# Performance work log

Measured on AMD Instinct MI355X. Metric: run time of the kernel, lower is better.

Reference implementation:

```python
import jax, jax.numpy as jnp
import numpy as np

H = 4096          # hidden_size
I = 11008         # intermediate_size
G = 128           # AWQ group_size
# AWQ interleaved nibble order within each packed int32
_ORDER = jnp.array([0, 4, 1, 5, 2, 6, 3, 7], dtype=jnp.int32) * 4


def _mk_lin(key, K, N):
    k1, k2, k3 = jax.random.split(key, 3)
    qw = jax.random.randint(k1, (K, N // 8), 0, 100, dtype=jnp.int32)
    qz = jax.random.randint(k2, (K // G, N // 8), 0, 100, dtype=jnp.int32)
    sc = jax.random.normal(k3, (K // G, N), dtype=jnp.float32) * 0.02
    return qw, qz, sc


def setup_inputs() -> dict:
    key = jax.random.key(0)
    ks = jax.random.split(key, 7)
    x = jax.random.normal(ks[0], (8, 16, H), dtype=jnp.float32)
    ln1_w = jnp.ones((H,), dtype=jnp.float32)
    ln2_w = jnp.ones((H,), dtype=jnp.float32)
    qkv_qw, qkv_qz, qkv_sc = _mk_lin(ks[1], H, 3 * H)
    o_qw, o_qz, o_sc = _mk_lin(ks[2], H, H)
    gu_qw, gu_qz, gu_sc = _mk_lin(ks[3], H, 2 * I)
    dn_qw, dn_qz, dn_sc = _mk_lin(ks[4], I, H)
    return dict(x=x, ln1_w=ln1_w, ln2_w=ln2_w,
                qkv_qw=qkv_qw, qkv_qz=qkv_qz, qkv_sc=qkv_sc,
                o_qw=o_qw, o_qz=o_qz, o_sc=o_sc,
                gu_qw=gu_qw, gu_qz=gu_qz, gu_sc=gu_sc,
                dn_qw=dn_qw, dn_qz=dn_qz, dn_sc=dn_sc)


def rmsnorm(x, w, eps=1e-6):
    return x * jax.lax.rsqrt(jnp.mean(x * x, axis=-1, keepdims=True) + eps) * w


def dequant(qw, qz, sc):
    # qw: [K, N//8] int32 -> [K, N]; qz: [K//G, N//8] -> [K//G, N]
    K = qw.shape[0]
    N = sc.shape[1]
    w = ((qw[:, :, None] >> _ORDER) & 0xF).reshape(K, N).astype(sc.dtype)
    z = ((qz[:, :, None] >> _ORDER) & 0xF).reshape(K // G, N).astype(sc.dtype)
    return (w - jnp.repeat(z, G, axis=0)) * jnp.repeat(sc, G, axis=0)


def lite_linear(x, qw, qz, sc):
    return x @ dequant(qw, qz, sc)


def reference(x, ln1_w, ln2_w,
              qkv_qw, qkv_qz, qkv_sc,
              o_qw, o_qz, o_sc,
              gu_qw, gu_qz, gu_sc,
              dn_qw, dn_qz, dn_sc):
    residual = x
    h = rmsnorm(x, ln1_w)
    h = lite_linear(h, qkv_qw, qkv_qz, qkv_sc)[..., :H]  # mock attn: take q slice
    h = lite_linear(h, o_qw, o_qz, o_sc)
    h = residual + h
    residual = h
    h = rmsnorm(h, ln2_w)
    gate_up = lite_linear(h, gu_qw, gu_qz, gu_sc)
    gate, up = gate_up[..., :I], gate_up[..., I:]
    h = lite_linear(jax.nn.silu(gate) * up, dn_qw, dn_qz, dn_sc)
    return residual + h
```

## Files before the change

kernel.cpp:

```cpp
#include <hip/hip_runtime.h>

typedef unsigned int   u32;
typedef unsigned short u16;

typedef _Float16 h2  __attribute__((ext_vector_type(2)));
typedef _Float16 h8  __attribute__((ext_vector_type(8)));
typedef float    f32x4 __attribute__((ext_vector_type(4)));

#define M_TOK 128

__device__ __forceinline__ u16 f2h_(float f) {
    _Float16 h = (_Float16)f; return __builtin_bit_cast(u16, h);
}
__device__ __forceinline__ float h2f_(u16 b) {
    _Float16 h = __builtin_bit_cast(_Float16, b); return (float)h;
}
__device__ __forceinline__ void acc8(uint4 v, float* s) {
#pragma unroll
    for (int i = 0; i < 4; ++i) {
        u32 w = ((const u32*)&v)[i];
        s[2 * i]     += h2f_((u16)(w & 0xFFFF));
        s[2 * i + 1] += h2f_((u16)(w >> 16));
    }
}

__constant__ int SHC[8] = {0, 16, 4, 20, 8, 24, 12, 28};

__launch_bounds__(256)
__global__ void pack_zs(const int* __restrict__ qz, const float* __restrict__ sc,
                        u32* __restrict__ zs, int qws, int scs, int Ncols, int total) {
    const int idx = blockIdx.x * 256 + threadIdx.x;
    if (idx >= total) return;
    const int g = idx / Ncols, n = idx - g * Ncols;
    const u32 d = (u32)qz[(size_t)g * qws + (n >> 3)];
    const u32 zj = (d >> SHC[n & 7]) & 15u;
    const u32 mz = 0xE400u | zj;
    const u16 sh = f2h_(sc[(size_t)g * scs + n]);
    zs[(size_t)g * Ncols + n] = mz | ((u32)sh << 16);
}


__launch_bounds__(256)
__global__ void rmsnorm_k(const float* __restrict__ in, const float* __restrict__ w,
                          u16* __restrict__ out) {
    const int row = blockIdx.x;
    const float* x = in + (size_t)row * 4096;
    float ss = 0.f;
#pragma unroll
    for (int j = 0; j < 16; ++j) {
        float v = x[threadIdx.x + 256 * j];
        ss += v * v;
    }
#pragma unroll
    for (int off = 32; off > 0; off >>= 1) ss += __shfl_down(ss, off, 64);
    __shared__ float ws4[4];
    if ((threadIdx.x & 63) == 0) ws4[threadIdx.x >> 6] = ss;
    __syncthreads();
    float total = ws4[0] + ws4[1] + ws4[2] + ws4[3];
    float r = rsqrtf(total * (1.f / 4096.f) + 1e-6f);
    const int mt = row >> 4, l16 = row & 15;
#pragma unroll
    for (int c2 = 0; c2 < 2; ++c2) {
        int c = threadIdx.x * 2 + c2;
        int kb = c >> 2, qq = c & 3;
        u16 o8[8];
#pragma unroll
        for (int j = 0; j < 8; ++j) {
            int i = c * 8 + j;
            o8[j] = f2h_(x[i] * r * w[i]);
        }
        *(uint4*)(out + ((size_t)(kb * 8 + mt) * 64 + qq * 16 + l16) * 8) = *(const uint4*)o8;
    }
}

__launch_bounds__(256, 3)
__global__ void gemm_awq(const u16* __restrict__ A, const u32* __restrict__ zs,
                         const int* __restrict__ qw, u16* __restrict__ part,
                         int qws, int N, int K, int kchunk) {
    __shared__ __align__(16) char lds[51200];

    const int tid = threadIdx.x, w = tid >> 6, lane = tid & 63;
    const int q = lane >> 4, l16 = lane & 15;
    const int nwg = gridDim.x, bid = blockIdx.x;
    const int qq8 = nwg >> 3, r8 = nwg & 7, xcd = bid & 7, boff = bid >> 3;
    const int bx = (xcd < r8 ? xcd * (qq8 + 1) : r8 * (qq8 + 1) + (xcd - r8) * qq8) + boff;
    const int n0w = bx * 128 + w * 32;
    const int pc0 = n0w >> 3;
    const int kp = lane & 31, h = lane >> 5;
    const int sk = blockIdx.y, kc0 = sk * kchunk, kend = min(kc0 + kchunk, K);

    char* ldsA0 = lds;
    char* ldsA1 = lds + 16384;
    char* myB   = lds + 32768 + w * 4608;
    const char* Ab = (const char*)A;
    const int stoff = w * 4096 + lane * 16;
    const int aoff  = (q * 16 + l16) * 16;
    const int* qws_base = qw + pc0;
    const u32* zsA = zs + n0w + h * 8;
    const u32* zsB = zs + n0w + 16 + h * 8;

    f32x4 acc[8][2] = {};
    uint4 za0, za1, zb0, zb1;

    auto ldraw = [&](int k0) -> uint4 {
        return *(const uint4*)(qws_base + (size_t)(k0 + lane) * qws);
    };
    auto loadzs = [&](int g) {
        za0 = *(const uint4*)(zsA + (size_t)g * N);
        za1 = *(const uint4*)(zsA + (size_t)g * N + 4);
        zb0 = *(const uint4*)(zsB + (size_t)g * N);
        zb1 = *(const uint4*)(zsB + (size_t)g * N + 4);
    };
    auto bperm8 = [&](uint4 rv, int* b) {
        const int i0 = kp * 8, i1 = i0 + 4;
        b[0] = __builtin_amdgcn_ds_bpermute(i0, (int)rv.x);
        b[1] = __builtin_amdgcn_ds_bpermute(i0, (int)rv.y);
        b[2] = __builtin_amdgcn_ds_bpermute(i0, (int)rv.z);
        b[3] = __builtin_amdgcn_ds_bpermute(i0, (int)rv.w);
        b[4] = __builtin_amdgcn_ds_bpermute(i1, (int)rv.x);
        b[5] = __builtin_amdgcn_ds_bpermute(i1, (int)rv.y);
        b[6] = __builtin_amdgcn_ds_bpermute(i1, (int)rv.z);
        b[7] = __builtin_amdgcn_ds_bpermute(i1, (int)rv.w);
    };
    auto emit_all = [&](const int* b, char* buf) {
        u32 qd0 = (u32)(h ? b[1] : b[0]);
        u32 qd1 = (u32)(h ? b[5] : b[4]);
        u32 qd2 = (u32)(h ? b[3] : b[2]);
        u32 qd3 = (u32)(h ? b[7] : b[6]);
        auto emit8 = [&](u32 w0, u32 w1, int nb, uint4 z0, uint4 z1) {
            char* bb = buf + kp * 4 + nb * 144;
            u32 w0s = w0 >> 4, w1s = w1 >> 4;
            auto em = [&](int j, u32 a0, u32 a1, int bsel, u32 zsj) {
                h2 mz = __builtin_bit_cast(h2, __builtin_amdgcn_perm(zsj, zsj, 0x01000100u));
                h2 s2 = __builtin_bit_cast(h2, __builtin_amdgcn_perm(zsj, zsj, 0x03020302u));
                u32 t = __builtin_amdgcn_perm(a1, a0, (u32)(bsel | ((bsel + 4) << 16)));
                u32 u = (t & 0x000F000Fu) | 0x64006400u;
                h2 v = (__builtin_bit_cast(h2, u) + mz) * s2;
                *(u32*)(bb + j * 144) = __builtin_bit_cast(u32, v);
            };
            em(0, w0, w1, 0, z0.x);  em(4, w0, w1, 1, z1.x);
            em(1, w0, w1, 2, z0.y);  em(5, w0, w1, 3, z1.y);
            em(2, w0s, w1s, 0, z0.z); em(6, w0s, w1s, 1, z1.z);
            em(3, w0s, w1s, 2, z0.w); em(7, w0s, w1s, 3, z1.w);
        };
        emit8(qd0, qd1, h * 8, za0, za1);
        emit8(qd2, qd3, 16 + h * 8, zb0, zb1);
    };

    loadzs(kc0 >> 7);
    uint4 rv0 = ldraw(kc0);
    uint4 rv_n = {0, 0, 0, 0};
    if (kc0 + 64 < kend) rv_n = ldraw(kc0 + 64);
    {
        const char* gs = Ab + (size_t)(kc0 >> 5) * 8192 + stoff;
        uint4 s0 = *(const uint4*)(gs);
        uint4 s1 = *(const uint4*)(gs + 1024);
        uint4 s2 = *(const uint4*)(gs + 2048);
        uint4 s3 = *(const uint4*)(gs + 3072);
        *(uint4*)(ldsA0 + stoff)        = s0;
        *(uint4*)(ldsA0 + stoff + 1024) = s1;
        *(uint4*)(ldsA0 + stoff + 2048) = s2;
        *(uint4*)(ldsA0 + stoff + 3072) = s3;
    }
    {
        int bp0[8];
        bperm8(rv0, bp0);
        emit_all(bp0, myB);
    }
    if (((kc0 + 64) & 127) == 0 && kc0 + 64 < kend)
        loadzs((kc0 + 64) >> 7);
    __syncthreads();

    char* cur = ldsA0; char* nxt = ldsA1;
    int bp[8];
    for (int k0 = kc0; k0 < kend; k0 += 64) {
        const bool kn1 = (k0 + 64) < kend, kn2 = (k0 + 128) < kend;
        uint4 s0 = {0,0,0,0}, s1 = {0,0,0,0}, s2 = {0,0,0,0}, s3 = {0,0,0,0};
        if (kn1) {
            const char* gs = Ab + (size_t)((k0 + 64) >> 5) * 8192 + stoff;
            s0 = *(const uint4*)(gs);
            s1 = *(const uint4*)(gs + 1024);
            s2 = *(const uint4*)(gs + 2048);
            s3 = *(const uint4*)(gs + 3072);
        }
        uint4 rv_f = {0, 0, 0, 0};
        if (kn2) rv_f = ldraw(k0 + 128);
        {
            uint4 bvc[2];
#pragma unroll
            for (int nt = 0; nt < 2; ++nt)
                bvc[nt] = *(const uint4*)(myB + (nt * 16 + l16) * 144 + q * 16);
            uint4 afc[8];
#pragma unroll
            for (int mt = 0; mt < 8; ++mt)
                afc[mt] = *(const uint4*)(cur + mt * 1024 + aoff);
            if (kn1) bperm8(rv_n, bp);
#pragma unroll
            for (int mt = 0; mt < 8; ++mt)
#pragma unroll
                for (int nt = 0; nt < 2; ++nt)
                    acc[mt][nt] = __builtin_amdgcn_mfma_f32_16x16x32_f16(
                        __builtin_bit_cast(h8, afc[mt]),
                        __builtin_bit_cast(h8, bvc[nt]),
                        acc[mt][nt], 0, 0, 0);
        }
        {
            uint4 bvc[2];
#pragma unroll
            for (int nt = 0; nt < 2; ++nt)
                bvc[nt] = *(const uint4*)(myB + (nt * 16 + l16) * 144 + 64 + q * 16);
            uint4 afc[8];
#pragma unroll
            for (int mt = 0; mt < 8; ++mt)
                afc[mt] = *(const uint4*)(cur + 8192 + mt * 1024 + aoff);
#pragma unroll
            for (int mt = 0; mt < 8; ++mt)
#pragma unroll
                for (int nt = 0; nt < 2; ++nt)
                    acc[mt][nt] = __builtin_amdgcn_mfma_f32_16x16x32_f16(
                        __builtin_bit_cast(h8, afc[mt]),
                        __builtin_bit_cast(h8, bvc[nt]),
                        acc[mt][nt], 0, 0, 0);
        }
        if (kn1) {
            emit_all(bp, myB);
            *(uint4*)(nxt + stoff)        = s0;
            *(uint4*)(nxt + stoff + 1024) = s1;
            *(uint4*)(nxt + stoff + 2048) = s2;
            *(uint4*)(nxt + stoff + 3072) = s3;
        }
        if (((k0 + 128) & 127) == 0 && (k0 + 128) < kend)
            loadzs((k0 + 128) >> 7);
        __syncthreads();
        rv_n = rv_f;
        char* t = cur; cur = nxt; nxt = t;
    }

    u16* pp = part + (size_t)sk * M_TOK * N;
#pragma unroll
    for (int mt = 0; mt < 8; ++mt)
#pragma unroll
        for (int nt = 0; nt < 2; ++nt) {
            const int n = n0w + nt * 16 + l16;
#pragma unroll
            for (int r = 0; r < 4; ++r) {
                const int m = mt * 16 + q * 4 + r;
                pp[(size_t)m * N + n] = f2h_(acc[mt][nt][r]);
            }
        }
}

__launch_bounds__(256)
__global__ void reduce_to_afrag(const u16* __restrict__ part, u16* __restrict__ out,
                                int SK) {
    const int idx = blockIdx.x * 256 + threadIdx.x;
    const int m = idx >> 9, c = idx & 511;
    float s[8] = {};
    for (int k = 0; k < SK; ++k)
        acc8(*(const uint4*)(part + (size_t)k * 524288 + (size_t)m * 4096 + c * 8), s);
    const int kb = c >> 2, qq = c & 3, mt = m >> 4, l16 = m & 15;
    u16 o8[8];
#pragma unroll
    for (int j = 0; j < 8; ++j) o8[j] = f2h_(s[j]);
    *(uint4*)(out + ((size_t)(kb * 8 + mt) * 64 + qq * 16 + l16) * 8) = *(const uint4*)o8;
}

__launch_bounds__(256)
__global__ void reduce_add_f32(const u16* __restrict__ part, const float* __restrict__ resin,
                               float* __restrict__ out, int SK) {
    const int idx = blockIdx.x * 256 + threadIdx.x;
    const size_t base = (size_t)idx * 8;
    float s[8];
    *(float4*)&s[0] = *(const float4*)(resin + base);
    *(float4*)&s[4] = *(const float4*)(resin + base + 4);
    for (int k = 0; k < SK; ++k)
        acc8(*(const uint4*)(part + (size_t)k * 524288 + base), s);
    *(float4*)(out + base)     = *(const float4*)&s[0];
    *(float4*)(out + base + 4) = *(const float4*)&s[4];
}

__launch_bounds__(256)
__global__ void silu_mul(const u16* __restrict__ part, u16* __restrict__ act, int SK) {
    const int idx = blockIdx.x * 256 + threadIdx.x;
    const int m = idx / 1376, c = idx - m * 1376;
    const int nb = c * 8;
    float g[8] = {}, u[8] = {};
    for (int k = 0; k < SK; ++k) {
        const size_t base = (size_t)k * 2818048 + (size_t)m * 22016 + nb;
        acc8(*(const uint4*)(part + base), g);
        acc8(*(const uint4*)(part + base + 11008), u);
    }
    const int kb = nb >> 5, qq = (nb >> 3) & 3, mt = m >> 4, l16 = m & 15;
    u16 o8[8];
#pragma unroll
    for (int j = 0; j < 8; ++j) {
        float a = g[j] / (1.f + __expf(-g[j])) * u[j];
        o8[j] = f2h_(a);
    }
    *(uint4*)(act + ((size_t)(kb * 8 + mt) * 64 + qq * 16 + l16) * 8) = *(const uint4*)o8;
}

extern "C" void kernel_launch(void* const* d_in, const int* in_sizes, int n_in,
                              void* d_out, int out_size, void* d_ws, size_t ws_size,
                              hipStream_t stream) {
    const float* x      = (const float*)d_in[0];
    const float* ln1_w  = (const float*)d_in[1];
    const float* ln2_w  = (const float*)d_in[2];
    const int*   qkv_qw = (const int*)d_in[3];
    const int*   qkv_qz = (const int*)d_in[4];
    const float* qkv_sc = (const float*)d_in[5];
    const int*   o_qw   = (const int*)d_in[6];
    const int*   o_qz   = (const int*)d_in[7];
    const float* o_sc   = (const float*)d_in[8];
    const int*   gu_qw  = (const int*)d_in[9];
    const int*   gu_qz  = (const int*)d_in[10];
    const float* gu_sc  = (const float*)d_in[11];
    const int*   dn_qw  = (const int*)d_in[12];
    const int*   dn_qz  = (const int*)d_in[13];
    const float* dn_sc  = (const float*)d_in[14];
    float* out = (float*)d_out;

    char* ws = (char*)d_ws;
    u16*   pbuf = (u16*)(ws);
    u32*   zsb  = (u32*)(ws + 45088768);
    u16*   act  = (u16*)(ws + 47906816);
    float* res2 = (float*)(ws + 50724864);
    u16*   slot = (u16*)(ws + 52822016);

    rmsnorm_k<<<128, 256, 0, stream>>>(x, ln1_w, slot);
    pack_zs<<<512, 256, 0, stream>>>(qkv_qz, qkv_sc, zsb, 1536, 12288, 4096, 131072);

    gemm_awq<<<dim3(32, 22), 256, 0, stream>>>(slot, zsb, qkv_qw, pbuf,
                                               1536, 4096, 4096, 192);
    reduce_to_afrag<<<256, 256, 0, stream>>>(pbuf, slot, 22);
    pack_zs<<<512, 256, 0, stream>>>(o_qz, o_sc, zsb, 512, 4096, 4096, 131072);

    gemm_awq<<<dim3(32, 22), 256, 0, stream>>>(slot, zsb, o_qw, pbuf,
                                               512, 4096, 4096, 192);
    reduce_add_f32<<<256, 256, 0, stream>>>(pbuf, x, res2, 22);

    rmsnorm_k<<<128, 256, 0, stream>>>(res2, ln2_w, slot);
    pack_zs<<<2752, 256, 0, stream>>>(gu_qz, gu_sc, zsb, 2752, 22016, 22016, 704512);

    gemm_awq<<<dim3(172, 5), 256, 0, stream>>>(slot, zsb, gu_qw, pbuf,
                                               2752, 22016, 4096, 832);
    silu_mul<<<688, 256, 0, stream>>>(pbuf, act, 5);
    pack_zs<<<1376, 256, 0, stream>>>(dn_qz, dn_sc, zsb, 512, 4096, 4096, 352256);

    gemm_awq<<<dim3(32, 25), 256, 0, stream>>>(act, zsb, dn_qw, pbuf,
                                               512, 4096, 11008, 448);
    reduce_add_f32<<<256, 256, 0, stream>>>(pbuf, res2, out, 25);
}
```

Before: 287.7 us.

## Halve AWQ GEMM K-step to 32, drop bpermute, raise occupancy to 4 waves

The AWQ GEMM main loop now advances K by 32 instead of 64. This halves the LDS footprint for the A double buffer and the dequantized B tile, so launch bounds can rise from 3 to 4 blocks per CU. Each lane now loads two scalar qweight words straight from global memory, replacing the uint4 load plus ds_bpermute shuffle, and the zero/scale registers shrink to one pair. The cost is twice as many loop iterations and __syncthreads barriers per K chunk, less MFMA work between barriers, and narrower, less coalesced qweight loads.

After: 304.7 us. 1.06x slower.

```diff
diff --git a/kernel.cpp b/kernel.cpp
--- a/kernel.cpp
+++ b/kernel.cpp
@@ -73,166 +73,113 @@
     }
 }
 
-__launch_bounds__(256, 3)
+__launch_bounds__(256, 4)
 __global__ void gemm_awq(const u16* __restrict__ A, const u32* __restrict__ zs,
                          const int* __restrict__ qw, u16* __restrict__ part,
                          int qws, int N, int K, int kchunk) {
-    __shared__ __align__(16) char lds[51200];
+    __shared__ __align__(16) char lds[25600];
 
     const int tid = threadIdx.x, w = tid >> 6, lane = tid & 63;
     const int q = lane >> 4, l16 = lane & 15;
+    const int kp = lane & 15, ho = lane >> 4;
     const int nwg = gridDim.x, bid = blockIdx.x;
     const int qq8 = nwg >> 3, r8 = nwg & 7, xcd = bid & 7, boff = bid >> 3;
     const int bx = (xcd < r8 ? xcd * (qq8 + 1) : r8 * (qq8 + 1) + (xcd - r8) * qq8) + boff;
     const int n0w = bx * 128 + w * 32;
     const int pc0 = n0w >> 3;
-    const int kp = lane & 31, h = lane >> 5;
     const int sk = blockIdx.y, kc0 = sk * kchunk, kend = min(kc0 + kchunk, K);
 
     char* ldsA0 = lds;
-    char* ldsA1 = lds + 16384;
-    char* myB   = lds + 32768 + w * 4608;
+    char* ldsA1 = lds + 8192;
+    char* myB   = lds + 16384 + w * 2304;
     const char* Ab = (const char*)A;
-    const int stoff = w * 4096 + lane * 16;
+    const int stoff = tid * 32;
     const int aoff  = (q * 16 + l16) * 16;
-    const int* qws_base = qw + pc0;
-    const u32* zsA = zs + n0w + h * 8;
-    const u32* zsB = zs + n0w + 16 + h * 8;
+    const int* qrow = qw + pc0 + ho;
+    const u32* zsP  = zs + n0w + ho * 8;
 
     f32x4 acc[8][2] = {};
-    uint4 za0, za1, zb0, zb1;
-
-    auto ldraw = [&](int k0) -> uint4 {
-        return *(const uint4*)(qws_base + (size_t)(k0 + lane) * qws);
+    uint4 z0, z1;
+
+    auto loadzs = [&](int g) {
+        z0 = *(const uint4*)(zsP + (size_t)g * N);
+        z1 = *(const uint4*)(zsP + (size_t)g * N + 4);
     };
-    auto loadzs = [&](int g) {
-        za0 = *(const uint4*)(zsA + (size_t)g * N);
-        za1 = *(const uint4*)(zsA + (size_t)g * N + 4);
-        zb0 = *(const uint4*)(zsB + (size_t)g * N);
-        zb1 = *(const uint4*)(zsB + (size_t)g * N + 4);
+    auto ldraw = [&](int k0, u32& d0, u32& d1) {
+        const size_t r = (size_t)(k0 + 2 * kp);
+        d0 = (u32)qrow[r * qws];
+        d1 = (u32)qrow[(r + 1) * qws];
     };
-    auto bperm8 = [&](uint4 rv, int* b) {
-        const int i0 = kp * 8, i1 = i0 + 4;
-        b[0] = __builtin_amdgcn_ds_bpermute(i0, (int)rv.x);
-        b[1] = __builtin_amdgcn_ds_bpermute(i0, (int)rv.y);
-        b[2] = __builtin_amdgcn_ds_bpermute(i0, (int)rv.z);
-        b[3] = __builtin_amdgcn_ds_bpermute(i0, (int)rv.w);
-        b[4] = __builtin_amdgcn_ds_bpermute(i1, (int)rv.x);
-        b[5] = __builtin_amdgcn_ds_bpermute(i1, (int)rv.y);
-        b[6] = __builtin_amdgcn_ds_bpermute(i1, (int)rv.z);
-        b[7] = __builtin_amdgcn_ds_bpermute(i1, (int)rv.w);
+    auto emit_all = [&](u32 a0, u32 a1) {
+        char* bb = myB + (size_t)ho * 576 + kp * 4;
+        u32 a0s = a0 >> 4, a1s = a1 >> 4;
+        auto em = [&](int j, u32 w0, u32 w1, int bsel, u32 zsj) {
+            h2 mz = __builtin_bit_cast(h2, __builtin_amdgcn_perm(zsj, zsj, 0x01000100u));
+            h2 s2 = __builtin_bit_cast(h2, __builtin_amdgcn_perm(zsj, zsj, 0x03020302u));
+            u32 t = __builtin_amdgcn_perm(w1, w0, (u32)(bsel | ((bsel + 4) << 16)));
+            u32 u = (t & 0x000F000Fu) | 0x64006400u;
+            h2 v = (__builtin_bit_cast(h2, u) + mz) * s2;
+            *(u32*)(bb + j * 72) = __builtin_bit_cast(u32, v);
+        };
+        em(0, a0, a1, 0, z0.x);   em(4, a0, a1, 1, z1.x);
+        em(1, a0, a1, 2, z0.y);   em(5, a0, a1, 3, z1.y);
+        em(2, a0s, a1s, 0, z0.z); em(6, a0s, a1s, 1, z1.z);
+        em(3, a0s, a1s, 2, z0.w); em(7, a0s, a1s, 3, z1.w);
     };
-    auto emit_all = [&](const int* b, char* buf) {
-        u32 qd0 = (u32)(h ? b[1] : b[0]);
-        u32 qd1 = (u32)(h ? b[5] : b[4]);
-        u32 qd2 = (u32)(h ? b[3] : b[2]);
-        u32 qd3 = (u32)(h ? b[7] : b[6]);
-        auto emit8 = [&](u32 w0, u32 w1, int nb, uint4 z0, uint4 z1) {
-            char* bb = buf + kp * 4 + nb * 144;
-            u32 w0s = w0 >> 4, w1s = w1 >> 4;
-            auto em = [&](int j, u32 a0, u32 a1, int bsel, u32 zsj) {
-                h2 mz = __builtin_bit_cast(h2, __builtin_amdgcn_perm(zsj, zsj, 0x01000100u));
-                h2 s2 = __builtin_bit_cast(h2, __builtin_amdgcn_perm(zsj, zsj, 0x03020302u));
-                u32 t = __builtin_amdgcn_perm(a1, a0, (u32)(bsel | ((bsel + 4) << 16)));
-                u32 u = (t & 0x000F000Fu) | 0x64006400u;
-                h2 v = (__builtin_bit_cast(h2, u) + mz) * s2;
-                *(u32*)(bb + j * 144) = __builtin_bit_cast(u32, v);
-            };
-            em(0, w0, w1, 0, z0.x);  em(4, w0, w1, 1, z1.x);
-            em(1, w0, w1, 2, z0.y);  em(5, w0, w1, 3, z1.y);
-            em(2, w0s, w1s, 0, z0.z); em(6, w0s, w1s, 1, z1.z);
-            em(3, w0s, w1s, 2, z0.w); em(7, w0s, w1s, 3, z1.w);
-        };
-        emit8(qd0, qd1, h * 8, za0, za1);
-        emit8(qd2, qd3, 16 + h * 8, zb0, zb1);
-    };
 
     loadzs(kc0 >> 7);
-    uint4 rv0 = ldraw(kc0);
-    uint4 rv_n = {0, 0, 0, 0};
-    if (kc0 + 64 < kend) rv_n = ldraw(kc0 + 64);
+    u32 e0, e1;
+    ldraw(kc0, e0, e1);
+    u32 rd0 = 0, rd1 = 0;
+    if (kc0 + 32 < kend) ldraw(kc0 + 32, rd0, rd1);
     {
         const char* gs = Ab + (size_t)(kc0 >> 5) * 8192 + stoff;
         uint4 s0 = *(const uint4*)(gs);
-        uint4 s1 = *(const uint4*)(gs + 1024);
-        uint4 s2 = *(const uint4*)(gs + 2048);
-        uint4 s3 = *(const uint4*)(gs + 3072);
-        *(uint4*)(ldsA0 + stoff)        = s0;
-        *(uint4*)(ldsA0 + stoff + 1024) = s1;
-        *(uint4*)(ldsA0 + stoff + 2048) = s2;
-        *(uint4*)(ldsA0 + stoff + 3072) = s3;
-    }
-    {
-        int bp0[8];
-        bperm8(rv0, bp0);
-        emit_all(bp0, myB);
-    }
-    if (((kc0 + 64) & 127) == 0 && kc0 + 64 < kend)
-        loadzs((kc0 + 64) >> 7);
+        uint4 s1 = *(const uint4*)(gs + 16);
+        *(uint4*)(ldsA0 + stoff)      = s0;
+        *(uint4*)(ldsA0 + stoff + 16) = s1;
+    }
+    emit_all(e0, e1);
     __syncthreads();
 
     char* cur = ldsA0; char* nxt = ldsA1;
-    int bp[8];
-    for (int k0 = kc0; k0 < kend; k0 += 64) {
-        const bool kn1 = (k0 + 64) < kend, kn2 = (k0 + 128) < kend;
-        uint4 s0 = {0,0,0,0}, s1 = {0,0,0,0}, s2 = {0,0,0,0}, s3 = {0,0,0,0};
+    for (int k0 = kc0; k0 < kend; k0 += 32) {
+        const bool kn1 = (k0 + 32) < kend, kn2 = (k0 + 64) < kend;
+        uint4 s0 = {0, 0, 0, 0}, s1 = {0, 0, 0, 0};
         if (kn1) {
-            const char* gs = Ab + (size_t)((k0 + 64) >> 5) * 8192 + stoff;
+            const char* gs = Ab + (size_t)((k0 + 32) >> 5) * 8192 + stoff;
             s0 = *(const uint4*)(gs);
-            s1 = *(const uint4*)(gs + 1024);
-            s2 = *(const uint4*)(gs + 2048);
-            s3 = *(const uint4*)(gs + 3072);
-        }
-        uint4 rv_f = {0, 0, 0, 0};
-        if (kn2) rv_f = ldraw(k0 + 128);
-        {
-            uint4 bvc[2];
-#pragma unroll
-            for (int nt = 0; nt < 2; ++nt)
-                bvc[nt] = *(const uint4*)(myB + (nt * 16 + l16) * 144 + q * 16);
-            uint4 afc[8];
-#pragma unroll
-            for (int mt = 0; mt < 8; ++mt)
-                afc[mt] = *(const uint4*)(cur + mt * 1024 + aoff);
-            if (kn1) bperm8(rv_n, bp);
-#pragma unroll
-            for (int mt = 0; mt < 8; ++mt)
-#pragma unroll
-                for (int nt = 0; nt < 2; ++nt)
-                    acc[mt][nt] = __builtin_amdgcn_mfma_f32_16x16x32_f16(
-                        __builtin_bit_cast(h8, afc[mt]),
-                        __builtin_bit_cast(h8, bvc[nt]),
-                        acc[mt][nt], 0, 0, 0);
-        }
-        {
-            uint4 bvc[2];
-#pragma unroll
-            for (int nt = 0; nt < 2; ++nt)
-                bvc[nt] = *(const uint4*)(myB + (nt * 16 + l16) * 144 + 64 + q * 16);
-            uint4 afc[8];
-#pragma unroll
-            for (int mt = 0; mt < 8; ++mt)
-                afc[mt] = *(const uint4*)(cur + 8192 + mt * 1024 + aoff);
-#pragma unroll
-            for (int mt = 0; mt < 8; ++mt)
-#pragma unroll
-                for (int nt = 0; nt < 2; ++nt)
-                    acc[mt][nt] = __builtin_amdgcn_mfma_f32_16x16x32_f16(
-                        __builtin_bit_cast(h8, afc[mt]),
-                        __builtin_bit_cast(h8, bvc[nt]),
-                        acc[mt][nt], 0, 0, 0);
-        }
+            s1 = *(const uint4*)(gs + 16);
+        }
+        u32 nd0 = 0, nd1 = 0;
+        if (kn2) ldraw(k0 + 64, nd0, nd1);
+        uint4 bv0 = *(const uint4*)(myB + l16 * 72 + q * 16);
+        uint4 bv1 = *(const uint4*)(myB + (16 + l16) * 72 + q * 16);
+#pragma unroll
+        for (int hh = 0; hh < 2; ++hh) {
+            uint4 afc[4];
+#pragma unroll
+            for (int mt = 0; mt < 4; ++mt)
+                afc[mt] = *(const uint4*)(cur + (size_t)(hh * 4 + mt) * 1024 + aoff);
+#pragma unroll
+            for (int mt = 0; mt < 4; ++mt) {
+                acc[hh * 4 + mt][0] = __builtin_amdgcn_mfma_f32_16x16x32_f16(
+                    __builtin_bit_cast(h8, afc[mt]), __builtin_bit_cast(h8, bv0),
+                    acc[hh * 4 + mt][0], 0, 0, 0);
+                acc[hh * 4 + mt][1] = __builtin_amdgcn_mfma_f32_16x16x32_f16(
+                    __builtin_bit_cast(h8, afc[mt]), __builtin_bit_cast(h8, bv1),
+                    acc[hh * 4 + mt][1], 0, 0, 0);
+            }
+        }
+        if (kn1 && (((k0 + 32) & 127) == 0))
+            loadzs((k0 + 32) >> 7);
         if (kn1) {
-            emit_all(bp, myB);
-            *(uint4*)(nxt + stoff)        = s0;
-            *(uint4*)(nxt + stoff + 1024) = s1;
-            *(uint4*)(nxt + stoff + 2048) = s2;
-            *(uint4*)(nxt + stoff + 3072) = s3;
-        }
-        if (((k0 + 128) & 127) == 0 && (k0 + 128) < kend)
-            loadzs((k0 + 128) >> 7);
+            emit_all(rd0, rd1);
+            *(uint4*)(nxt + stoff)      = s0;
+            *(uint4*)(nxt + stoff + 16) = s1;
+        }
         __syncthreads();
-        rv_n = rv_f;
+        rd0 = nd0; rd1 = nd1;
         char* t = cur; cur = nxt; nxt = t;
     }
 
```
